# Optimization experiments

Measured on AMD Instinct MI355X. Metric: run time of the kernel, lower is better.

Reference implementation:

```python
import jax, jax.numpy as jnp
import numpy as np

B, L, D, H = 4, 512, 256, 128  # batch, seq_len, input_size, hidden_size
NEG = -1e30


def setup_inputs() -> dict:
    key = jax.random.key(0)
    ks = jax.random.split(key, 16)
    init = lambda k, shape, fan_in: (jax.random.normal(k, shape, jnp.float32) / np.sqrt(fan_in).astype(np.float32))
    v = jax.random.normal(ks[0], (B, L, D), jnp.float32)
    lengths = jax.random.randint(ks[1], (B,), L // 2, L + 1).astype(jnp.int32)
    p_mask = (jnp.arange(L)[None, :] < lengths[:, None])  # [B, L] bool
    return {
        "v": v,
        "lengths": lengths,
        "p_mask": p_mask,
        "own_W": init(ks[2], (H, D), D), "own_b": jnp.zeros((H,), jnp.float32),
        "comp_W": init(ks[3], (H, D), D), "comp_b": jnp.zeros((H,), jnp.float32),
        "v_attn": init(ks[4], (H,), H),
        "gate_W": init(ks[5], (2 * D, 2 * D), 2 * D), "gate_b": jnp.zeros((2 * D,), jnp.float32),
        "w_ih_f": init(ks[6], (3 * H, 2 * D), 2 * D), "w_hh_f": init(ks[7], (3 * H, H), H),
        "b_ih_f": jnp.zeros((3 * H,), jnp.float32), "b_hh_f": jnp.zeros((3 * H,), jnp.float32),
        "w_ih_b": init(ks[8], (3 * H, 2 * D), 2 * D), "w_hh_b": init(ks[9], (3 * H, H), H),
        "b_ih_b": jnp.zeros((3 * H,), jnp.float32), "b_hh_b": jnp.zeros((3 * H,), jnp.float32),
    }


def _gru(x, tmask, w_ih, w_hh, b_ih, b_hh, reverse):
    """Single-direction GRU over [B, L, In] with length masking (emulates packing)."""
    Bn, Ln, _ = x.shape
    Hn = w_hh.shape[1]
    xp = jnp.einsum('bli,hi->blh', x, w_ih) + b_ih  # [B, L, 3H] input projections

    def step(h, inputs):
        xpt, m = inputs  # [B, 3H], [B, 1]
        hp = h @ w_hh.T + b_hh
        xr, xz, xn = jnp.split(xpt, 3, axis=-1)
        hr, hz, hn = jnp.split(hp, 3, axis=-1)
        r = jax.nn.sigmoid(xr + hr)
        z = jax.nn.sigmoid(xz + hz)
        n = jnp.tanh(xn + r * hn)
        h_new = (1.0 - z) * n + z * h
        h = jnp.where(m, h_new, h)
        return h, jnp.where(m, h_new, jnp.zeros_like(h_new))

    h0 = jnp.zeros((Bn, Hn), x.dtype)
    xs = (jnp.swapaxes(xp, 0, 1), tmask.T[:, :, None])
    _, outs = jax.lax.scan(step, h0, xs, reverse=reverse)
    return jnp.swapaxes(outs, 0, 1)  # [B, L, H]


def reference(v, lengths, p_mask, own_W, own_b, comp_W, comp_b, v_attn,
              gate_W, gate_b, w_ih_f, w_hh_f, b_ih_f, b_hh_f,
              w_ih_b, w_hh_b, b_ih_b, b_hh_b):
    # Additive (Bahdanau / RNet) self-attention, vectorized over all query positions.
    own = v @ own_W.T + own_b    # [B, L, H] (query term)
    comp = v @ comp_W.T + comp_b  # [B, L, H] (key term)
    # scores[b, q, k] = tanh(own_q + comp_k) . v_attn
    scores = jnp.einsum('bqkh,h->bqk', jnp.tanh(own[:, :, None, :] + comp[:, None, :, :]), v_attn)
    scores = jnp.where(p_mask[:, None, :], scores, NEG)  # mask padded keys
    attn = jax.nn.softmax(scores, axis=2)
    C = jnp.einsum('bqk,bkd->bqd', attn, v)  # attended context
    inp = jnp.concatenate([v, C], axis=-1)   # [B, L, 2D]
    inp = jax.nn.sigmoid(inp @ gate_W.T + gate_b) * inp  # gating
    # Bidirectional GRU encoder (pack_padded emulated via time mask; eval mode, no dropout).
    tmask = (jnp.arange(inp.shape[1])[None, :] < lengths[:, None])
    out_f = _gru(inp, tmask, w_ih_f, w_hh_f, b_ih_f, b_hh_f, reverse=False)
    out_b = _gru(inp, tmask, w_ih_b, w_hh_b, b_ih_b, b_hh_b, reverse=True)
    return jnp.concatenate([out_f, out_b], axis=-1)  # [B, L, 2H]
```

## Files before the change

### kernel.cpp

```cpp
#include <hip/hip_runtime.h>
#include <hip/hip_bf16.h>

#define NEGINF -1e30f

typedef __attribute__((ext_vector_type(8))) short short8;
typedef __attribute__((ext_vector_type(4))) float f32x4;

__device__ __forceinline__ float fast_sigmoid(float x) {
    return __builtin_amdgcn_rcpf(1.f + __expf(-x));
}
__device__ __forceinline__ float fast_tanh(float x) {
    return 1.f - 2.f * __builtin_amdgcn_rcpf(1.f + __expf(2.f * x));
}
__device__ __forceinline__ short f2bf(float f) {
    unsigned u = __float_as_uint(f);
    return (short)((u + 0x7fff + ((u >> 16) & 1)) >> 16);
}
__device__ __forceinline__ float bf2f(short b) {
    return __uint_as_float(((unsigned)(unsigned short)b) << 16);
}

__device__ __forceinline__ void bar_lds() {
    asm volatile("s_waitcnt lgkmcnt(0)\n\ts_barrier" ::: "memory");
}

__global__ __launch_bounds__(256) void gemm_bias(
    const float* __restrict__ A,
    const float* __restrict__ W1, const float* __restrict__ b1, float* __restrict__ out1,
    const float* __restrict__ W2, const float* __restrict__ b2, float* __restrict__ out2,
    const int* __restrict__ lengths,
    int M, int N, int K, int nsplit, int mode) {
    const int m0 = blockIdx.y * 64;
    if ((m0 & 511) >= lengths[m0 >> 9]) return;
    __shared__ __align__(16) short Abh[2][2048];
    __shared__ __align__(16) short Abl[2][2048];
    __shared__ __align__(16) short Bbh[2][2048];
    __shared__ __align__(16) short Bbl[2][2048];
    const int tid = threadIdx.x;
    int bx = blockIdx.x;
    const float* W = W1; const float* bias = b1; float* out = out1;
    int n0;
    if (bx < nsplit) {
        n0 = bx * 64;
    } else {
        W = W2; bias = b2; out = out2;
        n0 = (bx - nsplit) * 64;
    }
    const int wave = tid >> 6;
    const int lane = tid & 63;
    const int mrow = lane & 15;
    const int quad = lane >> 4;
    const int wm = (wave >> 1) * 32;
    const int wn = (wave & 1) * 32;

    const int r_ = tid >> 2;
    const int sg = (tid & 3) * 8;

    f32x4 acc[2][2];
#pragma unroll
    for (int mt = 0; mt < 2; mt++)
#pragma unroll
        for (int nt = 0; nt < 2; nt++) acc[mt][nt] = (f32x4){0.f, 0.f, 0.f, 0.f};

    float4 a0 = *(const float4*)(A + (size_t)(m0 + r_) * K + sg);
    float4 a1 = *(const float4*)(A + (size_t)(m0 + r_) * K + sg + 4);
    float4 w0 = *(const float4*)(W + (size_t)(n0 + r_) * K + sg);
    float4 w1 = *(const float4*)(W + (size_t)(n0 + r_) * K + sg + 4);

    for (int k0 = 0; k0 < K; k0 += 32) {
        const int cur = (k0 >> 5) & 1;
        {
            float av[8] = {a0.x, a0.y, a0.z, a0.w, a1.x, a1.y, a1.z, a1.w};
            float wv[8] = {w0.x, w0.y, w0.z, w0.w, w1.x, w1.y, w1.z, w1.w};
            short8 ah, al, bh, bl;
#pragma unroll
            for (int j = 0; j < 8; j++) {
                short h = f2bf(av[j]); ah[j] = h; al[j] = f2bf(av[j] - bf2f(h));
                short g = f2bf(wv[j]); bh[j] = g; bl[j] = f2bf(wv[j] - bf2f(g));
            }
            *(short8*)&Abh[cur][r_ * 32 + sg] = ah;
            *(short8*)&Abl[cur][r_ * 32 + sg] = al;
            *(short8*)&Bbh[cur][r_ * 32 + sg] = bh;
            *(short8*)&Bbl[cur][r_ * 32 + sg] = bl;
        }
        if (k0 + 32 < K) {
            a0 = *(const float4*)(A + (size_t)(m0 + r_) * K + k0 + 32 + sg);
            a1 = *(const float4*)(A + (size_t)(m0 + r_) * K + k0 + 32 + sg + 4);
            w0 = *(const float4*)(W + (size_t)(n0 + r_) * K + k0 + 32 + sg);
            w1 = *(const float4*)(W + (size_t)(n0 + r_) * K + k0 + 32 + sg + 4);
        }
        bar_lds();
        short8 Ah[2], Al[2], Bh[2], Bl[2];
#pragma unroll
        for (int t = 0; t < 2; t++) {
            int ar = (wm + t * 16 + mrow) * 32 + quad * 8;
            int br = (wn + t * 16 + mrow) * 32 + quad * 8;
            Ah[t] = *(const short8*)&Abh[cur][ar];
            Al[t] = *(const short8*)&Abl[cur][ar];
            Bh[t] = *(const short8*)&Bbh[cur][br];
            Bl[t] = *(const short8*)&Bbl[cur][br];
        }
#pragma unroll
        for (int mt = 0; mt < 2; mt++)
#pragma unroll
            for (int nt = 0; nt < 2; nt++) {
                acc[mt][nt] = __builtin_amdgcn_mfma_f32_16x16x32_bf16(Ah[mt], Bh[nt], acc[mt][nt], 0, 0, 0);
                acc[mt][nt] = __builtin_amdgcn_mfma_f32_16x16x32_bf16(Al[mt], Bh[nt], acc[mt][nt], 0, 0, 0);
                acc[mt][nt] = __builtin_amdgcn_mfma_f32_16x16x32_bf16(Ah[mt], Bl[nt], acc[mt][nt], 0, 0, 0);
            }
        bar_lds();
    }
    float bsv[2];
#pragma unroll
    for (int nt = 0; nt < 2; nt++) bsv[nt] = bias[n0 + wn + nt * 16 + mrow];
#pragma unroll
    for (int mt = 0; mt < 2; mt++)
#pragma unroll
        for (int nt = 0; nt < 2; nt++) {
            int n = n0 + wn + nt * 16 + mrow;
#pragma unroll
            for (int r = 0; r < 4; r++) {
                int m = m0 + wm + mt * 16 + quad * 4 + r;
                float val = acc[mt][nt][r] + bsv[nt];
                if (mode == 1) val = fast_sigmoid(val) * A[(size_t)m * K + n];
                out[(size_t)m * N + n] = val;
            }
        }
}

__global__ __launch_bounds__(512) void attn_kernel(
    const float* __restrict__ v, const int* __restrict__ lengths,
    const float* __restrict__ own, const float* __restrict__ comp,
    const float* __restrict__ v_attn, float* __restrict__ inp) {
    const int L = 512, D = 256, H = 128;
    const int b = blockIdx.x >> 6;
    const int q0 = (blockIdx.x & 63) * 8;
    const int len = lengths[b];
    if (q0 >= len) return;
    const int tid = threadIdx.x;
    const float K2E = 2.8853900817779268f;
    __shared__ __align__(16) float oKT[128 * 8];
    __shared__ float va2s[128];
    __shared__ __align__(16) float scf[512 * 12];
    __shared__ float inv8[8];

    for (int i = tid; i < 1024; i += 512) {
        int qq = i >> 7, hh = i & 127;
        oKT[hh * 8 + qq] = K2E * own[((size_t)(b * L + q0 + qq)) * H + hh];
    }
    if (tid < 128) va2s[tid] = -2.f * v_attn[tid];
    __syncthreads();

    {
        const int k = tid;
        float acc[8];
#pragma unroll
        for (int q = 0; q < 8; q++) acc[q] = 0.f;
        if (k < len) {
            const float* cp = comp + ((size_t)(b * L + k)) * H;
            for (int h = 0; h < 128; h += 4) {
                float4 c4 = *(const float4*)(cp + h);
                const float* cv = (const float*)&c4;
#pragma unroll
                for (int j = 0; j < 4; j++) {
                    float cK = cv[j] * K2E;
                    float va = va2s[h + j];
                    float4 o0 = *(const float4*)&oKT[(h + j) * 8];
                    float4 o1 = *(const float4*)&oKT[(h + j) * 8 + 4];
                    const float* op0 = (const float*)&o0;
                    const float* op1 = (const float*)&o1;
#pragma unroll
                    for (int q = 0; q < 4; q++) {
                        float r = __builtin_amdgcn_rcpf(1.f + exp2f(cK + op0[q]));
                        acc[q] = fmaf(va, r, acc[q]);
                    }
#pragma unroll
                    for (int q = 0; q < 4; q++) {
                        float r = __builtin_amdgcn_rcpf(1.f + exp2f(cK + op1[q]));
                        acc[4 + q] = fmaf(va, r, acc[4 + q]);
                    }
                }
            }
#pragma unroll
            for (int q = 0; q < 8; q++) acc[q] = __expf(acc[q]);
        }
        *(float4*)&scf[k * 12] = *(float4*)&acc[0];
        *(float4*)&scf[k * 12 + 4] = *(float4*)&acc[4];
    }
    __syncthreads();

    {
        int w = tid >> 6, l = tid & 63;
        float s = 0.f;
#pragma unroll
        for (int kk = 0; kk < 8; kk++) s += scf[(l + kk * 64) * 12 + w];
#pragma unroll
        for (int off = 1; off < 64; off <<= 1) s += __shfl_xor(s, off);
        if (l == 0) inv8[w] = __builtin_amdgcn_rcpf(s);
    }
    __syncthreads();

    {
        const int d = tid & 255;
        const int qh = tid >> 8;
        float c0 = 0.f, c1 = 0.f, c2 = 0.f, c3 = 0.f;
        const float* vb = v + ((size_t)b * L) * D + d;
        for (int k = 0; k < L; k += 2) {
            float v0 = vb[(size_t)k * D];
            float v1 = vb[(size_t)(k + 1) * D];
            float4 s0 = *(const float4*)&scf[k * 12 + qh * 4];
            float4 s1 = *(const float4*)&scf[(k + 1) * 12 + qh * 4];
            c0 += s0.x * v0 + s1.x * v1;
            c1 += s0.y * v0 + s1.y * v1;
            c2 += s0.z * v0 + s1.z * v1;
            c3 += s0.w * v0 + s1.w * v1;
        }
        float cc[4] = {c0, c1, c2, c3};
#pragma unroll
        for (int j = 0; j < 4; j++) {
            int q = q0 + qh * 4 + j;
            size_t row = ((size_t)(b * L + q)) * 512;
            inp[row + 256 + d] = cc[j] * inv8[qh * 4 + j];
            inp[row + d] = v[((size_t)(b * L + q)) * D + d];
        }
    }
}

__global__ __launch_bounds__(512, 1) void gru_kernel(
    const float* __restrict__ xp_f, const float* __restrict__ xp_b,
    const float* __restrict__ w_hh_f, const float* __restrict__ w_hh_b,
    const float* __restrict__ b_hh_f, const float* __restrict__ b_hh_b,
    const int* __restrict__ lengths, float* __restrict__ out) {
    const int L = 512, H = 128;
    const int dir = blockIdx.x >> 2;
    const int b = blockIdx.x & 3;
    const float* xp = dir ? xp_b : xp_f;
    const float* w_hh = dir ? w_hh_b : w_hh_f;
    const float* b_hh = dir ? b_hh_b : b_hh_f;
    const int tid = threadIdx.x;
    const int wave = tid >> 6;
    const int lane = tid & 63;
    const int mrow = lane & 15;
    const int quad = lane >> 4;
    const int jj = 16 * wave + lane;

    __shared__ __align__(16) short hbuf[2][320];

    short8 wb[3][4];
#pragma unroll
    for (int g = 0; g < 3; g++) {
        int row = g * 128 + 16 * wave + mrow;
#pragma unroll
        for (int kt = 0; kt < 4; kt++) {
            const float* wp = w_hh + (size_t)row * H + kt * 32 + quad * 8;
            float4 w0 = *(const float4*)(wp);
            float4 w1 = *(const float4*)(wp + 4);
            float wv[8] = {w0.x, w0.y, w0.z, w0.w, w1.x, w1.y, w1.z, w1.w};
            short8 hi8;
#pragma unroll
            for (int k = 0; k < 8; k++) hi8[k] = f2bf(wv[k]);
            wb[g][kt] = hi8;
        }
    }
    float br = 0.f, bz = 0.f, bn = 0.f, hcur = 0.f;
    if (lane < 16) {
        br = b_hh[jj];
        bz = b_hh[128 + jj];
        bn = b_hh[256 + jj];
    }

    const int len = lengths[b];
    for (int i = tid; i < (L - len) * 128; i += 512) {
        int tt = len + (i >> 7);
        int kk = i & 127;
        out[((size_t)(b * L + tt)) * 256 + dir * 128 + kk] = 0.f;
    }
    if (tid < 320) hbuf[0][tid] = 0;

    const int nch = (len + 15) >> 4;
    float xr[16], xz[16], xn[16];
    if (lane < 16) {
#pragma unroll
        for (int s = 0; s < 16; s++) {
            if (s < len) {
                int t = dir ? (len - 1 - s) : s;
                size_t base = ((size_t)(b * L + t)) * 384;
                xr[s] = xp[base + jj];
                xz[s] = xp[base + 128 + jj];
                xn[s] = xp[base + 256 + jj];
            }
        }
    }
    __syncthreads();

    const int bbase = ((mrow & 1) ? 160 : 0) + quad * 8;
    int par = 0;

    for (int c = 0; c < nch; c++) {
        const int cnt = min(16, len - c * 16);
        float nxr[16], nxz[16], nxn[16];
        if (lane < 16 && c + 1 < nch) {
#pragma unroll
            for (int s = 0; s < 16; s++) {
                int rr = (c + 1) * 16 + s;
                if (rr < len) {
                    int t = dir ? (len - 1 - rr) : rr;
                    size_t base = ((size_t)(b * L + t)) * 384;
                    nxr[s] = xp[base + jj];
                    nxz[s] = xp[base + 128 + jj];
                    nxn[s] = xp[base + 256 + jj];
                }
            }
        }
#pragma unroll
        for (int s = 0; s < 16; s++) {
            if (s < cnt) {
                short8 af[4];
#pragma unroll
                for (int kt = 0; kt < 4; kt++)
                    af[kt] = *(const short8*)&hbuf[par][bbase + kt * 32];
                f32x4 acc[3];
#pragma unroll
                for (int g = 0; g < 3; g++) acc[g] = (f32x4){0.f, 0.f, 0.f, 0.f};
#pragma unroll
                for (int kt = 0; kt < 4; kt++)
#pragma unroll
                    for (int g = 0; g < 3; g++)
                        acc[g] = __builtin_amdgcn_mfma_f32_16x16x32_bf16(af[kt], wb[g][kt], acc[g], 0, 0, 0);
                if (lane < 16) {
                    float hr = acc[0][0] + acc[0][1] + br;
                    float hz = acc[1][0] + acc[1][1] + bz;
                    float hh = acc[2][0] + acc[2][1] + bn;
                    float r = fast_sigmoid(xr[s] + hr);
                    float z = fast_sigmoid(xz[s] + hz);
                    float n = fast_tanh(xn[s] + r * hh);
                    float hn = (1.f - z) * n + z * hcur;
                    hcur = hn;
                    short hb = f2bf(hn);
                    hbuf[par ^ 1][jj] = hb;
                    hbuf[par ^ 1][160 + jj] = f2bf(hn - bf2f(hb));
                    int t = dir ? (len - 1 - (c * 16 + s)) : (c * 16 + s);
                    out[((size_t)(b * L + t)) * 256 + dir * 128 + jj] = hn;
                }
                par ^= 1;
                bar_lds();
            }
        }
        if (lane < 16 && c + 1 < nch) {
#pragma unroll
            for (int s = 0; s < 16; s++) { xr[s] = nxr[s]; xz[s] = nxz[s]; xn[s] = nxn[s]; }
        }
    }
}

extern "C" void kernel_launch(void* const* d_in, const int* in_sizes, int n_in,
                              void* d_out, int out_size, void* d_ws, size_t ws_size,
                              hipStream_t stream) {
    const int B = 4, L = 512, D = 256, H = 128;
    const int M = B * L;

    const float* v      = (const float*)d_in[0];
    const int* lengths  = (const int*)d_in[1];
    const float* own_W  = (const float*)d_in[3];
    const float* own_b  = (const float*)d_in[4];
    const float* comp_W = (const float*)d_in[5];
    const float* comp_b = (const float*)d_in[6];
    const float* v_attn = (const float*)d_in[7];
    const float* gate_W = (const float*)d_in[8];
    const float* gate_b = (const float*)d_in[9];
    const float* w_ih_f = (const float*)d_in[10];
    const float* w_hh_f = (const float*)d_in[11];
    const float* b_ih_f = (const float*)d_in[12];
    const float* b_hh_f = (const float*)d_in[13];
    const float* w_ih_b = (const float*)d_in[14];
    const float* w_hh_b = (const float*)d_in[15];
    const float* b_ih_b = (const float*)d_in[16];
    const float* b_hh_b = (const float*)d_in[17];

    float* ws   = (float*)d_ws;
    float* own  = ws;
    float* comp = own + (size_t)M * H;
    float* inp  = comp + (size_t)M * H;
    float* gated = inp + (size_t)M * 512;
    float* xp_f = gated + (size_t)M * 512;
    float* xp_b = xp_f + (size_t)M * 384;
    float* out  = (float*)d_out;

    gemm_bias<<<dim3(4, M / 64), 256, 0, stream>>>(
        v, own_W, own_b, own, comp_W, comp_b, comp, lengths, M, H, D, 2, 0);
    attn_kernel<<<dim3(B * 64), 512, 0, stream>>>(v, lengths, own, comp, v_attn, inp);
    gemm_bias<<<dim3(8, M / 64), 256, 0, stream>>>(
        inp, gate_W, gate_b, gated, gate_W, gate_b, gated, lengths, M, 512, 512, 8, 1);
    gemm_bias<<<dim3(12, M / 64), 256, 0, stream>>>(
        gated, w_ih_f, b_ih_f, xp_f, w_ih_b, b_ih_b, xp_b, lengths, M, 384, 512, 6, 0);
    gru_kernel<<<dim3(8), 512, 0, stream>>>(xp_f, xp_b, w_hh_f, w_hh_b, b_hh_f, b_hh_b, lengths, out);
}
```

Measured before the change: 384.4 us.

## Quantize GRU recurrent matmul to int8 MFMA with split hidden-state encoding

Replaces the bf16 hi/lo split recurrent matmul with an int8 path. W_hh is quantized per gate-row with a max-abs scale, and the hidden state is encoded as a 13-bit fixed-point value split into two int8 halves. The step then uses 16x16x64 i8 MFMAs, six per step instead of twelve bf16 ones, to shorten the serial latency of each timestep. This lowers weight precision to int8 per-row quantization, which may raise numerical error over 512 recurrent steps.

```diff
diff --git a/kernel.cpp b/kernel.cpp
--- a/kernel.cpp
+++ b/kernel.cpp
@@ -5,6 +5,7 @@
 
 typedef __attribute__((ext_vector_type(8))) short short8;
 typedef __attribute__((ext_vector_type(4))) float f32x4;
+typedef __attribute__((ext_vector_type(4))) int int4_t;
 
 __device__ __forceinline__ float fast_sigmoid(float x) {
     return __builtin_amdgcn_rcpf(1.f + __expf(-x));
@@ -244,22 +245,41 @@
     const int quad = lane >> 4;
     const int jj = 16 * wave + lane;
 
-    __shared__ __align__(16) short hbuf[2][320];
-
-    short8 wb[3][4];
+    __shared__ __align__(16) signed char hbufc[2][384];
+
+    int4_t wb[3][2];
+    float ws[3];
 #pragma unroll
     for (int g = 0; g < 3; g++) {
         int row = g * 128 + 16 * wave + mrow;
-#pragma unroll
-        for (int kt = 0; kt < 4; kt++) {
-            const float* wp = w_hh + (size_t)row * H + kt * 32 + quad * 8;
-            float4 w0 = *(const float4*)(wp);
-            float4 w1 = *(const float4*)(wp + 4);
-            float wv[8] = {w0.x, w0.y, w0.z, w0.w, w1.x, w1.y, w1.z, w1.w};
-            short8 hi8;
-#pragma unroll
-            for (int k = 0; k < 8; k++) hi8[k] = f2bf(wv[k]);
-            wb[g][kt] = hi8;
+        float wv[32];
+#pragma unroll
+        for (int kt = 0; kt < 2; kt++)
+#pragma unroll
+            for (int j4 = 0; j4 < 4; j4++) {
+                float4 f4 = *(const float4*)(w_hh + (size_t)row * H + kt * 64 + quad * 16 + j4 * 4);
+                wv[kt * 16 + j4 * 4 + 0] = f4.x;
+                wv[kt * 16 + j4 * 4 + 1] = f4.y;
+                wv[kt * 16 + j4 * 4 + 2] = f4.z;
+                wv[kt * 16 + j4 * 4 + 3] = f4.w;
+            }
+        float mx = 0.f;
+#pragma unroll
+        for (int j = 0; j < 32; j++) mx = fmaxf(mx, fabsf(wv[j]));
+        mx = fmaxf(mx, __shfl_xor(mx, 16));
+        mx = fmaxf(mx, __shfl_xor(mx, 32));
+        mx = fmaxf(mx, 1e-30f);
+        float inv_s = 127.f / mx;
+        ws[g] = (mx / 127.f) * (1.f / 8192.f);
+#pragma unroll
+        for (int kt = 0; kt < 2; kt++) {
+            int tmp[4] = {0, 0, 0, 0};
+#pragma unroll
+            for (int j = 0; j < 16; j++) {
+                int q = (int)rintf(wv[kt * 16 + j] * inv_s);
+                tmp[j >> 2] |= (q & 0xff) << ((j & 3) * 8);
+            }
+            wb[g][kt] = (int4_t){tmp[0], tmp[1], tmp[2], tmp[3]};
         }
     }
     float br = 0.f, bz = 0.f, bn = 0.f, hcur = 0.f;
@@ -275,7 +295,7 @@
         int kk = i & 127;
         out[((size_t)(b * L + tt)) * 256 + dir * 128 + kk] = 0.f;
     }
-    if (tid < 320) hbuf[0][tid] = 0;
+    for (int i = tid; i < 768; i += 512) ((signed char*)hbufc)[i] = 0;
 
     const int nch = (len + 15) >> 4;
     float xr[16], xz[16], xn[16];
@@ -293,7 +313,7 @@
     }
     __syncthreads();
 
-    const int bbase = ((mrow & 1) ? 160 : 0) + quad * 8;
+    const int bbase = ((mrow & 1) ? 192 : 0) + quad * 16;
     int par = 0;
 
     for (int c = 0; c < nch; c++) {
@@ -315,30 +335,30 @@
 #pragma unroll
         for (int s = 0; s < 16; s++) {
             if (s < cnt) {
-                short8 af[4];
-#pragma unroll
-                for (int kt = 0; kt < 4; kt++)
-                    af[kt] = *(const short8*)&hbuf[par][bbase + kt * 32];
-                f32x4 acc[3];
-#pragma unroll
-                for (int g = 0; g < 3; g++) acc[g] = (f32x4){0.f, 0.f, 0.f, 0.f};
-#pragma unroll
-                for (int kt = 0; kt < 4; kt++)
-#pragma unroll
-                    for (int g = 0; g < 3; g++)
-                        acc[g] = __builtin_amdgcn_mfma_f32_16x16x32_bf16(af[kt], wb[g][kt], acc[g], 0, 0, 0);
+                int4_t af0 = *(const int4_t*)&hbufc[par][bbase];
+                int4_t af1 = *(const int4_t*)&hbufc[par][bbase + 64];
+                int4_t a0 = (int4_t){0, 0, 0, 0};
+                int4_t a1 = (int4_t){0, 0, 0, 0};
+                int4_t a2 = (int4_t){0, 0, 0, 0};
+                a0 = __builtin_amdgcn_mfma_i32_16x16x64_i8(af0, wb[0][0], a0, 0, 0, 0);
+                a0 = __builtin_amdgcn_mfma_i32_16x16x64_i8(af1, wb[0][1], a0, 0, 0, 0);
+                a1 = __builtin_amdgcn_mfma_i32_16x16x64_i8(af0, wb[1][0], a1, 0, 0, 0);
+                a1 = __builtin_amdgcn_mfma_i32_16x16x64_i8(af1, wb[1][1], a1, 0, 0, 0);
+                a2 = __builtin_amdgcn_mfma_i32_16x16x64_i8(af0, wb[2][0], a2, 0, 0, 0);
+                a2 = __builtin_amdgcn_mfma_i32_16x16x64_i8(af1, wb[2][1], a2, 0, 0, 0);
                 if (lane < 16) {
-                    float hr = acc[0][0] + acc[0][1] + br;
-                    float hz = acc[1][0] + acc[1][1] + bz;
-                    float hh = acc[2][0] + acc[2][1] + bn;
-                    float r = fast_sigmoid(xr[s] + hr);
-                    float z = fast_sigmoid(xz[s] + hz);
+                    float r = fast_sigmoid(fmaf((float)(a0[0] * 64 + a0[1]), ws[0], xr[s] + br));
+                    float z = fast_sigmoid(fmaf((float)(a1[0] * 64 + a1[1]), ws[1], xz[s] + bz));
+                    float hh = fmaf((float)(a2[0] * 64 + a2[1]), ws[2], bn);
                     float n = fast_tanh(xn[s] + r * hh);
                     float hn = (1.f - z) * n + z * hcur;
                     hcur = hn;
-                    short hb = f2bf(hn);
-                    hbuf[par ^ 1][jj] = hb;
-                    hbuf[par ^ 1][160 + jj] = f2bf(hn - bf2f(hb));
+                    float hs = fminf(fmaxf(hn * 8192.f, -8191.f), 8191.f);
+                    int h13 = (int)rintf(hs);
+                    int hi = h13 >> 6;
+                    int lo = h13 - (hi << 6);
+                    hbufc[par ^ 1][jj] = (signed char)hi;
+                    hbufc[par ^ 1][192 + jj] = (signed char)lo;
                     int t = dir ? (len - 1 - (c * 16 + s)) : (c * 16 + s);
                     out[((size_t)(b * L + t)) * 256 + dir * 128 + jj] = hn;
                 }
```

Result: faster. 354.1 us (-7.9%).
